# Kernel tuning notes

Measured on AMD Instinct MI355X. Metric: run time of the kernel, lower is better.

## Reference

```python
import jax, jax.numpy as jnp
import numpy as np

LENGTH = 512
Q = 2 * LENGTH + 3  # num_states = 2*length + 3
ALPHA = 26          # amino-acid alphabet size
BATCH = 256
T = 512


def setup_inputs() -> dict:
    key = jax.random.key(0)
    k1, k2, k3, k4 = jax.random.split(key, 4)
    x = jax.random.randint(k1, (BATCH, T), 0, ALPHA, dtype=jnp.int32)
    A_logits = jax.random.normal(k2, (Q, Q), dtype=jnp.float32)
    B_logits = jax.random.normal(k3, (Q, ALPHA), dtype=jnp.float32)
    init_logits = jax.random.normal(k4, (Q,), dtype=jnp.float32)
    return {"x": x, "A_logits": A_logits, "B_logits": B_logits, "init_logits": init_logits}


def reference(x, A_logits, B_logits, init_logits):
    # Build stochastic matrices (as emitter/transitioner do from their kernels).
    A = jax.nn.softmax(A_logits, axis=-1)        # (q, q) row-stochastic transitions
    B = jax.nn.softmax(B_logits, axis=-1)        # (q, alpha) emission distributions
    init = jax.nn.softmax(init_logits)           # (q,) initial distribution

    # Precompute per-position emission probs: E[b, t, :] = B[:, x[b, t]]
    E = B.T[x]                                   # (B, T, q)

    # First step (self.init branch): forward = E0 * initial distribution
    f0 = E[:, 0] * init[None, :]                 # (B, q)
    S0 = jnp.sum(f0, axis=-1, keepdims=True)     # (B, 1)
    ll0 = jnp.log(S0)
    f0 = f0 / S0

    def step(carry, Et):
        f, ll = carry
        fwd = Et * (f @ A)                       # emit * transition  (B, q)
        S = jnp.sum(fwd, axis=-1, keepdims=True)
        ll = ll + jnp.log(S)
        fwd = fwd / S
        return (fwd, ll), fwd

    (_, loglik), fwd_seq = jax.lax.scan(step, (f0, ll0), jnp.swapaxes(E[:, 1:], 0, 1))
    # fwd_seq: (T-1, B, q) -> full (B, T, q) with first step prepended
    forward = jnp.swapaxes(jnp.concatenate([f0[None], fwd_seq], axis=0), 0, 1)
    return forward, loglik
```

## Files before the change

### kernel.cpp

```cpp
#include <hip/hip_runtime.h>
#include <stdint.h>


#define Q     1027
#define TT    512
#define ALPH  26
#define KCH   33
#define NTILE 65
#define NCHK  (KCH*64)
#define GIMG  (NCHK*16)
#define NCL   16
#define WPC   16
#define MB    16

typedef short  short8  __attribute__((ext_vector_type(8)));
typedef float  floatx4 __attribute__((ext_vector_type(4)));
typedef int    intx4   __attribute__((ext_vector_type(4)));

static constexpr size_t al512(size_t x) { return (x + 511) & ~size_t(511); }
static constexpr size_t OFF_APACK = 0;
static constexpr size_t SZ_APACK  = (size_t)NTILE * KCH * 64 * 16;
static constexpr size_t OFF_BSOFT = al512(OFF_APACK + SZ_APACK);
static constexpr size_t SZ_BSOFT  = (size_t)Q * ALPH * 4;
static constexpr size_t OFF_INIT  = al512(OFF_BSOFT + SZ_BSOFT);
static constexpr size_t OFF_AMAX  = al512(OFF_INIT + Q * 4);
static constexpr size_t OFF_AINV  = al512(OFF_AMAX + Q * 4);
static constexpr size_t OFF_GEX   = al512(OFF_AINV + Q * 4);
static constexpr size_t SZ_GEX    = (size_t)NCL * 2 * GIMG;
static constexpr size_t OFF_SP    = al512(OFF_GEX + SZ_GEX);
static constexpr size_t SZ_SP     = (size_t)NCL * 2 * 64 * MB * 4;
static constexpr size_t OFF_FLAGS = al512(OFF_SP + SZ_SP);
static constexpr size_t SZ_FLAGS  = (size_t)NCL * 64 * 4;
static constexpr size_t WS_NEED   = OFF_FLAGS + SZ_FLAGS;
static constexpr size_t FWDSZ     = (size_t)256 * TT * Q;

__device__ __forceinline__ uint32_t f2bf(float f) {
  uint32_t u = __float_as_uint(f);
  return (u + 0x7fffu + ((u >> 16) & 1u)) >> 16;
}


__global__ void k_zero(char* __restrict__ ws) {
  const size_t n = (WS_NEED - OFF_GEX) / 16;
  intx4* p = (intx4*)(ws + OFF_GEX);
  for (size_t i = (size_t)blockIdx.x * 256 + threadIdx.x; i < n; i += (size_t)80 * 256)
    p[i] = intx4{0, 0, 0, 0};
}

__global__ void k_astats(const float* __restrict__ A, char* __restrict__ ws) {
  const int r = blockIdx.x, tid = threadIdx.x;
  const float* row = A + (size_t)r * Q;
  __shared__ float red[4], red2[4];
  float mx = -3.0e38f;
  for (int i = tid; i < Q; i += 256) mx = fmaxf(mx, row[i]);
#pragma unroll
  for (int d = 1; d < 64; d <<= 1) mx = fmaxf(mx, __shfl_xor(mx, d));
  if ((tid & 63) == 0) red[tid >> 6] = mx;
  __syncthreads();
  mx = fmaxf(fmaxf(red[0], red[1]), fmaxf(red[2], red[3]));
  float s = 0.f;
  for (int i = tid; i < Q; i += 256) s += expf(row[i] - mx);
#pragma unroll
  for (int d = 1; d < 64; d <<= 1) s += __shfl_xor(s, d);
  if ((tid & 63) == 0) red2[tid >> 6] = s;
  __syncthreads();
  s = red2[0] + red2[1] + red2[2] + red2[3];
  if (tid == 0) {
    *(float*)(ws + OFF_AMAX + (size_t)r * 4) = mx;
    *(float*)(ws + OFF_AINV + (size_t)r * 4) = 1.0f / s;
  }
}

__global__ void k_bsoft(const float* __restrict__ Bl, char* __restrict__ ws) {
  const int r = blockIdx.x, l = threadIdx.x;
  float v = (l < ALPH) ? Bl[(size_t)r * ALPH + l] : -3.0e38f;
  float mx = v;
#pragma unroll
  for (int d = 1; d < 64; d <<= 1) mx = fmaxf(mx, __shfl_xor(mx, d));
  float e = (l < ALPH) ? expf(v - mx) : 0.f;
  float s = e;
#pragma unroll
  for (int d = 1; d < 64; d <<= 1) s += __shfl_xor(s, d);
  if (l < ALPH) *(float*)(ws + OFF_BSOFT + ((size_t)r * ALPH + l) * 4) = e / s;
}

__global__ void k_isoft(const float* __restrict__ il, char* __restrict__ ws) {
  const int tid = threadIdx.x;
  __shared__ float red[4], red2[4];
  float mx = -3.0e38f;
  for (int i = tid; i < Q; i += 256) mx = fmaxf(mx, il[i]);
#pragma unroll
  for (int d = 1; d < 64; d <<= 1) mx = fmaxf(mx, __shfl_xor(mx, d));
  if ((tid & 63) == 0) red[tid >> 6] = mx;
  __syncthreads();
  mx = fmaxf(fmaxf(red[0], red[1]), fmaxf(red[2], red[3]));
  float s = 0.f;
  for (int i = tid; i < Q; i += 256) s += expf(il[i] - mx);
#pragma unroll
  for (int d = 1; d < 64; d <<= 1) s += __shfl_xor(s, d);
  if ((tid & 63) == 0) red2[tid >> 6] = s;
  __syncthreads();
  s = red2[0] + red2[1] + red2[2] + red2[3];
  const float inv = 1.0f / s;
  for (int i = tid; i < Q; i += 256)
    *(float*)(ws + OFF_INIT + (size_t)i * 4) = expf(il[i] - mx) * inv;
}

__global__ void k_repack(const float* __restrict__ A, char* __restrict__ ws) {
  const int b = blockIdx.x;
  const int nt = b % NTILE, kc = b / NTILE;
  const int lane = threadIdx.x;
  const int q = nt * 16 + (lane & 15);
  const int kb = kc * 32 + (lane >> 4) * 8;
  union { short8 v; unsigned short u[8]; } pk;
#pragma unroll
  for (int e = 0; e < 8; ++e) {
    const int k = kb + e;
    float val = 0.f;
    if (k < Q && q < Q) {
      const float mxk = *(const float*)(ws + OFF_AMAX + (size_t)k * 4);
      const float ivk = *(const float*)(ws + OFF_AINV + (size_t)k * 4);
      val = expf(A[(size_t)k * Q + q] - mxk) * ivk;
    }
    pk.u[e] = (unsigned short)f2bf(val);
  }
  *(short8*)(ws + OFF_APACK + (((size_t)nt * KCH + kc) * 64 + lane) * 16) = pk.v;
}


__global__ __launch_bounds__(256, 1) void k_main(const int* __restrict__ xin,
                                                 char* __restrict__ ws,
                                                 float* __restrict__ out) {
  const int bid = blockIdx.x;
  const int c = bid & 15, j = bid >> 4;
  const int tid = threadIdx.x;
  const int lane = tid & 63, w = tid >> 6;
  const int cL = lane & 15, g4 = lane >> 4;
  const int tg = 4 * j + w;
  const bool jx = (j == 15), two = (jx && w == 3);
  const uint64_t wsu = (uint64_t)(uintptr_t)ws;

  __shared__ floatx4 accx[4][5][64];
  __shared__ uint8_t x_lds[MB * TT];
  __shared__ float   B_lds[5][16][ALPH];
  __shared__ float   init_lds[5][16];
  __shared__ float   SpW[4][16];

  for (int idx = tid; idx < MB * TT; idx += 256)
    x_lds[idx] = (uint8_t)xin[(size_t)(c * MB) * TT + idx];
  for (int idx = tid; idx < 5 * 16 * ALPH; idx += 256) {
    const int tl = idx / (16 * ALPH), rem = idx % (16 * ALPH);
    const int cc = rem / ALPH, a = rem % ALPH;
    const int grow = (tl < 4 ? 64 * j + tl * 16 : 1024) + cc;
    B_lds[tl][cc][a] = (grow < Q) ? *(const float*)(ws + OFF_BSOFT + ((size_t)grow * ALPH + a) * 4) : 0.f;
  }
  for (int idx = tid; idx < 5 * 16; idx += 256) {
    const int tl = idx / 16, cc = idx % 16;
    const int grow = (tl < 4 ? 64 * j + tl * 16 : 1024) + cc;
    init_lds[tl][cc] = (grow < Q) ? *(const float*)(ws + OFF_INIT + (size_t)grow * 4) : 0.f;
  }

  short8 af[4][9];
#pragma unroll
  for (int tt = 0; tt < 4; ++tt)
#pragma unroll
    for (int i = 0; i < 9; ++i)
      if (i < 8 || w == 0)
        af[tt][i] = *(const short8*)(ws + OFF_APACK +
                      (((size_t)(4 * j + tt) * KCH + (4 * i + w)) * 64 + lane) * 16);
  short8 afx[9];
  if (jx) {
#pragma unroll
    for (int i = 0; i < 9; ++i)
      if (i < 8 || w == 0)
        afx[i] = *(const short8*)(ws + OFF_APACK +
                      (((size_t)64 * KCH + (4 * i + w)) * 64 + lane) * 16);
  }
  __syncthreads();

  float up0[4], upx[4] = {0.f, 0.f, 0.f, 0.f};
  float uold[4], uxold[4] = {0.f, 0.f, 0.f, 0.f};
  float llacc = 0.f;

#define POST_STEP(TCUR)                                                                   \
  do {                                                                                    \
    const int par_ = (TCUR) & 1;                                                          \
    const uint64_t gb_ = wsu + OFF_GEX + (size_t)(c * 2 + par_) * GIMG;                   \
    const uint64_t b0_ = gb_ + (size_t)((tg >> 1) * 1024 + ((tg & 1) * 2 + (cL >> 3)) * 256 \
                         + g4 * 64 + (cL & 7) * 2);                                       \
    float t0_ = up0[0], t1_ = up0[1], t2_ = up0[2], t3_ = up0[3];                         \
    _Pragma("unroll") for (int r = 0; r < 4; ++r) {                                       \
      uint32_t v0_ = f2bf(up0[r]);                                                        \
      asm volatile("global_store_short %0, %1, off sc0 sc1" ::                            \
                   "v"(b0_ + (size_t)(r * 16)), "v"(v0_) : "memory");                     \
    }                                                                                     \
    if (two) {                                                                            \
      const uint64_t bx_ = gb_ + (size_t)(32 * 1024 + (cL >> 3) * 256 + g4 * 64 +         \
                           (cL & 7) * 2);                                                 \
      _Pragma("unroll") for (int r = 0; r < 4; ++r) {                                     \
        uint32_t v1_ = f2bf(upx[r]);                                                      \
        asm volatile("global_store_short %0, %1, off sc0 sc1" ::                          \
                     "v"(bx_ + (size_t)(r * 16)), "v"(v1_) : "memory");                   \
      }                                                                                   \
      t0_ += upx[0]; t1_ += upx[1]; t2_ += upx[2]; t3_ += upx[3];                         \
    }                                                                                     \
    _Pragma("unroll") for (int d = 1; d < 16; d <<= 1) {                                  \
      t0_ += __shfl_xor(t0_, d); t1_ += __shfl_xor(t1_, d);                               \
      t2_ += __shfl_xor(t2_, d); t3_ += __shfl_xor(t3_, d);                               \
    }                                                                                     \
    if (cL == 0) {                                                                        \
      floatx4 sv_; sv_[0] = t0_; sv_[1] = t1_; sv_[2] = t2_; sv_[3] = t3_;                \
      uint64_t sa_ = wsu + OFF_SP + (size_t)(c * 2 + par_) * 4096 +                       \
                     (size_t)(tg * 64 + g4 * 16);                                         \
      asm volatile("global_store_dwordx4 %0, %1, off sc0 sc1" :: "v"(sa_), "v"(sv_)       \
                   : "memory");                                                           \
    }                                                                                     \
    asm volatile("s_waitcnt vmcnt(0)" ::: "memory");                                      \
    __builtin_amdgcn_sched_barrier(0);                                                    \
    if (lane == 0) {                                                                      \
      int fv_ = (TCUR) + 1;                                                               \
      asm volatile("global_store_dword %0, %1, off sc0 sc1" ::                            \
                   "v"(wsu + OFF_FLAGS + (size_t)(c * 64 + tg) * 4), "v"(fv_) : "memory");\
    }                                                                                     \
  } while (0)

#define WAIT_FLAGS(TGT)                                                                   \
  do {                                                                                    \
    if (w == 0) {                                                                         \
      const uint64_t fa_ = wsu + OFF_FLAGS + (size_t)(c * 64 + lane) * 4;                 \
      for (;;) {                                                                          \
        int f_;                                                                           \
        asm volatile("global_load_dword %0, %1, off sc0 sc1\n\ts_waitcnt vmcnt(0)"        \
                     : "=v"(f_) : "v"(fa_) : "memory");                                   \
        if (__all(f_ >= (TGT))) break;                                                    \
        __builtin_amdgcn_s_sleep(2);                                                      \
      }                                                                                   \
    }                                                                                     \
    __syncthreads();                                                                      \
  } while (0)

#pragma unroll
  for (int r = 0; r < 4; ++r) {
    const int m = g4 * 4 + r;
    const int xm = x_lds[m * TT + 0];
    up0[r] = B_lds[w][cL][xm] * init_lds[w][cL];
    uold[r] = up0[r];
    if (two) { upx[r] = B_lds[4][cL][xm] * init_lds[4][cL]; uxold[r] = upx[r]; }
  }
  POST_STEP(0);

  for (int t = 1; t < TT; ++t) {
    const int parp = (t - 1) & 1;
    WAIT_FLAGS(t);

    const uint64_t gb = wsu + OFF_GEX + (size_t)(c * 2 + parp) * GIMG;
    intx4 sg[9], spi;
#pragma unroll
    for (int i = 0; i < 8; ++i)
      asm volatile("global_load_dwordx4 %0, %1, off sc0 sc1"
                   : "=v"(sg[i]) : "v"(gb + (size_t)((i * 256 + tid) * 16)) : "memory");
    if (w == 0)
      asm volatile("global_load_dwordx4 %0, %1, off sc0 sc1"
                   : "=v"(sg[8]) : "v"(gb + (size_t)((2048 + lane) * 16)) : "memory");
    asm volatile("global_load_dwordx4 %0, %1, off sc0 sc1"
                 : "=v"(spi)
                 : "v"(wsu + OFF_SP + (size_t)(c * 2 + parp) * 4096 + (size_t)tid * 16)
                 : "memory");
    asm volatile("s_waitcnt vmcnt(1)" ::: "memory");
    __builtin_amdgcn_sched_barrier(0);

    floatx4 acc[4] = {{0,0,0,0},{0,0,0,0},{0,0,0,0},{0,0,0,0}};
    floatx4 acx = {0, 0, 0, 0};
#pragma unroll
    for (int i = 0; i < 8; ++i) {
      const short8 gf = __builtin_bit_cast(short8, sg[i]);
#pragma unroll
      for (int tt = 0; tt < 4; ++tt)
        acc[tt] = __builtin_amdgcn_mfma_f32_16x16x32_bf16(gf, af[tt][i], acc[tt], 0, 0, 0);
      if (jx) acx = __builtin_amdgcn_mfma_f32_16x16x32_bf16(gf, afx[i], acx, 0, 0, 0);
    }
    if (w == 0) {
      const short8 gf = __builtin_bit_cast(short8, sg[8]);
#pragma unroll
      for (int tt = 0; tt < 4; ++tt)
        acc[tt] = __builtin_amdgcn_mfma_f32_16x16x32_bf16(gf, af[tt][8], acc[tt], 0, 0, 0);
      if (jx) acx = __builtin_amdgcn_mfma_f32_16x16x32_bf16(gf, afx[8], acx, 0, 0, 0);
    }
#pragma unroll
    for (int tt = 0; tt < 4; ++tt) accx[w][tt][lane] = acc[tt];
    if (jx) accx[w][4][lane] = acx;

    asm volatile("s_waitcnt vmcnt(0)" ::: "memory");
    __builtin_amdgcn_sched_barrier(0);
    floatx4 s4 = __builtin_bit_cast(floatx4, spi);
#pragma unroll
    for (int d = 4; d < 64; d <<= 1) {
#pragma unroll
      for (int e = 0; e < 4; ++e) s4[e] += __shfl_xor(s4[e], d);
    }
    if (lane < 4) *(floatx4*)&SpW[w][lane * 4] = s4;
    __syncthreads();

    float invS[4], ot0[4], ot1[4];
    floatx4 rs = accx[0][w][lane] + accx[1][w][lane] + accx[2][w][lane] + accx[3][w][lane];
    float rx[4];
    if (two) {
      floatx4 q = accx[0][4][lane] + accx[1][4][lane] + accx[2][4][lane] + accx[3][4][lane];
#pragma unroll
      for (int r = 0; r < 4; ++r) rx[r] = q[r];
    }
#pragma unroll
    for (int r = 0; r < 4; ++r) {
      const int m = g4 * 4 + r;
      invS[r] = 1.0f / (SpW[0][m] + SpW[1][m] + SpW[2][m] + SpW[3][m]);
      ot0[r] = uold[r] * invS[r];
      if (two) ot1[r] = uxold[r] * invS[r];
      const int xm = x_lds[m * TT + t];
      up0[r] = rs[r] * B_lds[w][cL][xm] * invS[r];
      uold[r] = up0[r];
      if (two) { upx[r] = rx[r] * B_lds[4][cL][xm] * invS[r]; uxold[r] = upx[r]; }
    }

    POST_STEP(t);

#pragma unroll
    for (int r = 0; r < 4; ++r) {
      const int m = g4 * 4 + r;
      const size_t ob = ((size_t)(c * MB + m) * TT + (t - 1)) * Q;
      __builtin_nontemporal_store(ot0[r], out + ob + tg * 16 + cL);
      if (two && cL < 3)
        __builtin_nontemporal_store(ot1[r], out + ob + 1024 + cL);
    }
    if (j == 0 && w == 0 && lane < 16)
      llacc += logf(SpW[0][lane] + SpW[1][lane] + SpW[2][lane] + SpW[3][lane]);
  }

  WAIT_FLAGS(TT);
  {
    const int parp = (TT - 1) & 1;
    intx4 spi;
    asm volatile("global_load_dwordx4 %0, %1, off sc0 sc1\n\ts_waitcnt vmcnt(0)"
                 : "=v"(spi)
                 : "v"(wsu + OFF_SP + (size_t)(c * 2 + parp) * 4096 + (size_t)tid * 16)
                 : "memory");
    __builtin_amdgcn_sched_barrier(0);
    floatx4 s4 = __builtin_bit_cast(floatx4, spi);
#pragma unroll
    for (int d = 4; d < 64; d <<= 1) {
#pragma unroll
      for (int e = 0; e < 4; ++e) s4[e] += __shfl_xor(s4[e], d);
    }
    if (lane < 4) *(floatx4*)&SpW[w][lane * 4] = s4;
    __syncthreads();
    float invS[4];
#pragma unroll
    for (int r = 0; r < 4; ++r) {
      const int m = g4 * 4 + r;
      invS[r] = 1.0f / (SpW[0][m] + SpW[1][m] + SpW[2][m] + SpW[3][m]);
    }
#pragma unroll
    for (int r = 0; r < 4; ++r) {
      const int m = g4 * 4 + r;
      const size_t ob = ((size_t)(c * MB + m) * TT + (TT - 1)) * Q;
      __builtin_nontemporal_store(up0[r] * invS[r], out + ob + tg * 16 + cL);
      if (two && cL < 3)
        __builtin_nontemporal_store(upx[r] * invS[r], out + ob + 1024 + cL);
    }
    if (j == 0 && w == 0 && lane < 16) {
      llacc += logf(SpW[0][lane] + SpW[1][lane] + SpW[2][lane] + SpW[3][lane]);
      out[FWDSZ + (size_t)c * MB + lane] = llacc;
    }
  }
}


extern "C" void kernel_launch(void* const* d_in, const int* in_sizes, int n_in,
                              void* d_out, int out_size, void* d_ws, size_t ws_size,
                              hipStream_t stream) {
  const int*   x    = (const int*)d_in[0];
  const float* Alog = (const float*)d_in[1];
  const float* Blog = (const float*)d_in[2];
  const float* ilog = (const float*)d_in[3];
  char*  ws  = (char*)d_ws;
  float* out = (float*)d_out;
  if (ws_size < WS_NEED) return;

  hipLaunchKernelGGL(k_zero,   dim3(80),          dim3(256), 0, stream, ws);
  hipLaunchKernelGGL(k_astats, dim3(Q),           dim3(256), 0, stream, Alog, ws);
  hipLaunchKernelGGL(k_bsoft,  dim3(Q),           dim3(64),  0, stream, Blog, ws);
  hipLaunchKernelGGL(k_isoft,  dim3(1),           dim3(256), 0, stream, ilog, ws);
  hipLaunchKernelGGL(k_repack, dim3(NTILE * KCH), dim3(64),  0, stream, Alog, ws);
  hipLaunchKernelGGL(k_main,   dim3(NCL * WPC),   dim3(256), 0, stream, x, ws, out);
}
```

Baseline: 2.152 ms.

## Derive row sums from the exchanged state buffer and prefetch flags early

Drops the separate per-tile partial-sum buffer and its global store and load. Each block now recomputes the normalisation sums by adding up the bf16 state vector it already loads from the exchange buffer. The flag poll is issued right after publishing, overlapping its latency, and the sleep is removed from the spin loop. This trims one global round trip and some cross-block traffic per step. In exchange it adds per-step unpacking arithmetic and sums rounded bf16 values instead of fp32 partials, which may change the normaliser slightly.

```diff
diff --git a/kernel.cpp b/kernel.cpp
--- a/kernel.cpp
+++ b/kernel.cpp
@@ -27,9 +27,7 @@
 static constexpr size_t OFF_AINV  = al512(OFF_AMAX + Q * 4);
 static constexpr size_t OFF_GEX   = al512(OFF_AINV + Q * 4);
 static constexpr size_t SZ_GEX    = (size_t)NCL * 2 * GIMG;
-static constexpr size_t OFF_SP    = al512(OFF_GEX + SZ_GEX);
-static constexpr size_t SZ_SP     = (size_t)NCL * 2 * 64 * MB * 4;
-static constexpr size_t OFF_FLAGS = al512(OFF_SP + SZ_SP);
+static constexpr size_t OFF_FLAGS = al512(OFF_GEX + SZ_GEX);
 static constexpr size_t SZ_FLAGS  = (size_t)NCL * 64 * 4;
 static constexpr size_t WS_NEED   = OFF_FLAGS + SZ_FLAGS;
 static constexpr size_t FWDSZ     = (size_t)256 * TT * Q;
@@ -39,11 +37,22 @@
   return (u + 0x7fffu + ((u >> 16) & 1u)) >> 16;
 }
 
+__device__ __forceinline__ float sum8(intx4 v) {
+  float s = 0.f;
+#pragma unroll
+  for (int e = 0; e < 4; ++e) {
+    const uint32_t u = (uint32_t)v[e];
+    s += __uint_as_float(u << 16);
+    s += __uint_as_float(u & 0xffff0000u);
+  }
+  return s;
+}
+
 
 __global__ void k_zero(char* __restrict__ ws) {
   const size_t n = (WS_NEED - OFF_GEX) / 16;
   intx4* p = (intx4*)(ws + OFF_GEX);
-  for (size_t i = (size_t)blockIdx.x * 256 + threadIdx.x; i < n; i += (size_t)80 * 256)
+  for (size_t i = (size_t)blockIdx.x * 256 + threadIdx.x; i < n; i += (size_t)72 * 256)
     p[i] = intx4{0, 0, 0, 0};
 }
 
@@ -139,12 +148,13 @@
   const int tg = 4 * j + w;
   const bool jx = (j == 15), two = (jx && w == 3);
   const uint64_t wsu = (uint64_t)(uintptr_t)ws;
+  const uint64_t outu = (uint64_t)(uintptr_t)out;
 
   __shared__ floatx4 accx[4][5][64];
   __shared__ uint8_t x_lds[MB * TT];
   __shared__ float   B_lds[5][16][ALPH];
   __shared__ float   init_lds[5][16];
-  __shared__ float   SpW[4][16];
+  __shared__ float   SpP[4][16];
 
   for (int idx = tid; idx < MB * TT; idx += 256)
     x_lds[idx] = (uint8_t)xin[(size_t)(c * MB) * TT + idx];
@@ -181,63 +191,31 @@
   float up0[4], upx[4] = {0.f, 0.f, 0.f, 0.f};
   float uold[4], uxold[4] = {0.f, 0.f, 0.f, 0.f};
   float llacc = 0.f;
-
-#define POST_STEP(TCUR)                                                                   \
+  const uint64_t fa = wsu + OFF_FLAGS + (size_t)(c * 64 + lane) * 4;
+  const uint64_t myfa = wsu + OFF_FLAGS + (size_t)(c * 64 + tg) * 4;
+
+#define POSTG(TCUR)                                                                       \
   do {                                                                                    \
     const int par_ = (TCUR) & 1;                                                          \
     const uint64_t gb_ = wsu + OFF_GEX + (size_t)(c * 2 + par_) * GIMG;                   \
     const uint64_t b0_ = gb_ + (size_t)((tg >> 1) * 1024 + ((tg & 1) * 2 + (cL >> 3)) * 256 \
                          + g4 * 64 + (cL & 7) * 2);                                       \
-    float t0_ = up0[0], t1_ = up0[1], t2_ = up0[2], t3_ = up0[3];                         \
-    _Pragma("unroll") for (int r = 0; r < 4; ++r) {                                       \
-      uint32_t v0_ = f2bf(up0[r]);                                                        \
+    _Pragma("unroll") for (int r_ = 0; r_ < 4; ++r_) {                                    \
+      uint32_t v_ = f2bf(up0[r_]);                                                        \
       asm volatile("global_store_short %0, %1, off sc0 sc1" ::                            \
-                   "v"(b0_ + (size_t)(r * 16)), "v"(v0_) : "memory");                     \
+                   "v"(b0_ + (size_t)(r_ * 16)), "v"(v_) : "memory");                     \
     }                                                                                     \
     if (two) {                                                                            \
-      const uint64_t bx_ = gb_ + (size_t)(32 * 1024 + (cL >> 3) * 256 + g4 * 64 +         \
-                           (cL & 7) * 2);                                                 \
-      _Pragma("unroll") for (int r = 0; r < 4; ++r) {                                     \
-        uint32_t v1_ = f2bf(upx[r]);                                                      \
+      const uint64_t bx_ = gb_ + (size_t)(32 * 1024 + (cL >> 3) * 256 + g4 * 64 + (cL & 7) * 2); \
+      _Pragma("unroll") for (int r_ = 0; r_ < 4; ++r_) {                                  \
+        uint32_t v_ = f2bf(upx[r_]);                                                      \
         asm volatile("global_store_short %0, %1, off sc0 sc1" ::                          \
-                     "v"(bx_ + (size_t)(r * 16)), "v"(v1_) : "memory");                   \
+                     "v"(bx_ + (size_t)(r_ * 16)), "v"(v_) : "memory");                   \
       }                                                                                   \
-      t0_ += upx[0]; t1_ += upx[1]; t2_ += upx[2]; t3_ += upx[3];                         \
-    }                                                                                     \
-    _Pragma("unroll") for (int d = 1; d < 16; d <<= 1) {                                  \
-      t0_ += __shfl_xor(t0_, d); t1_ += __shfl_xor(t1_, d);                               \
-      t2_ += __shfl_xor(t2_, d); t3_ += __shfl_xor(t3_, d);                               \
-    }                                                                                     \
-    if (cL == 0) {                                                                        \
-      floatx4 sv_; sv_[0] = t0_; sv_[1] = t1_; sv_[2] = t2_; sv_[3] = t3_;                \
-      uint64_t sa_ = wsu + OFF_SP + (size_t)(c * 2 + par_) * 4096 +                       \
-                     (size_t)(tg * 64 + g4 * 16);                                         \
-      asm volatile("global_store_dwordx4 %0, %1, off sc0 sc1" :: "v"(sa_), "v"(sv_)       \
-                   : "memory");                                                           \
-    }                                                                                     \
-    asm volatile("s_waitcnt vmcnt(0)" ::: "memory");                                      \
-    __builtin_amdgcn_sched_barrier(0);                                                    \
-    if (lane == 0) {                                                                      \
-      int fv_ = (TCUR) + 1;                                                               \
-      asm volatile("global_store_dword %0, %1, off sc0 sc1" ::                            \
-                   "v"(wsu + OFF_FLAGS + (size_t)(c * 64 + tg) * 4), "v"(fv_) : "memory");\
     }                                                                                     \
   } while (0)
 
-#define WAIT_FLAGS(TGT)                                                                   \
-  do {                                                                                    \
-    if (w == 0) {                                                                         \
-      const uint64_t fa_ = wsu + OFF_FLAGS + (size_t)(c * 64 + lane) * 4;                 \
-      for (;;) {                                                                          \
-        int f_;                                                                           \
-        asm volatile("global_load_dword %0, %1, off sc0 sc1\n\ts_waitcnt vmcnt(0)"        \
-                     : "=v"(f_) : "v"(fa_) : "memory");                                   \
-        if (__all(f_ >= (TGT))) break;                                                    \
-        __builtin_amdgcn_s_sleep(2);                                                      \
-      }                                                                                   \
-    }                                                                                     \
-    __syncthreads();                                                                      \
-  } while (0)
+  int f;
 
 #pragma unroll
   for (int r = 0; r < 4; ++r) {
@@ -247,14 +225,27 @@
     uold[r] = up0[r];
     if (two) { upx[r] = B_lds[4][cL][xm] * init_lds[4][cL]; uxold[r] = upx[r]; }
   }
-  POST_STEP(0);
+  POSTG(0);
+  asm volatile("global_load_dword %0, %1, off sc0 sc1" : "=v"(f) : "v"(fa) : "memory");
+  asm volatile("s_waitcnt vmcnt(0)" ::: "memory");
+  __builtin_amdgcn_sched_barrier(0);
+  if (lane == 0) {
+    int fv = 1;
+    asm volatile("global_store_dword %0, %1, off sc0 sc1" :: "v"(myfa), "v"(fv) : "memory");
+  }
 
   for (int t = 1; t < TT; ++t) {
     const int parp = (t - 1) & 1;
-    WAIT_FLAGS(t);
+
+    for (;;) {
+      if (__all(f >= t)) break;
+      asm volatile("global_load_dword %0, %1, off sc0 sc1\n\ts_waitcnt vmcnt(0)"
+                   : "=v"(f) : "v"(fa) : "memory");
+    }
+    __builtin_amdgcn_sched_barrier(0);
 
     const uint64_t gb = wsu + OFF_GEX + (size_t)(c * 2 + parp) * GIMG;
-    intx4 sg[9], spi;
+    intx4 sg[9];
 #pragma unroll
     for (int i = 0; i < 8; ++i)
       asm volatile("global_load_dwordx4 %0, %1, off sc0 sc1"
@@ -262,12 +253,16 @@
     if (w == 0)
       asm volatile("global_load_dwordx4 %0, %1, off sc0 sc1"
                    : "=v"(sg[8]) : "v"(gb + (size_t)((2048 + lane) * 16)) : "memory");
-    asm volatile("global_load_dwordx4 %0, %1, off sc0 sc1"
-                 : "=v"(spi)
-                 : "v"(wsu + OFF_SP + (size_t)(c * 2 + parp) * 4096 + (size_t)tid * 16)
-                 : "memory");
-    asm volatile("s_waitcnt vmcnt(1)" ::: "memory");
+    asm volatile("s_waitcnt vmcnt(0)" ::: "memory");
     __builtin_amdgcn_sched_barrier(0);
+
+    float ps = 0.f;
+#pragma unroll
+    for (int i = 0; i < 8; ++i) ps += sum8(sg[i]);
+    if (w == 0) ps += sum8(sg[8]);
+    ps += __shfl_xor(ps, 16);
+    ps += __shfl_xor(ps, 32);
+    if (lane < 16) SpP[w][lane] = ps;
 
     floatx4 acc[4] = {{0,0,0,0},{0,0,0,0},{0,0,0,0},{0,0,0,0}};
     floatx4 acx = {0, 0, 0, 0};
@@ -290,15 +285,6 @@
     for (int tt = 0; tt < 4; ++tt) accx[w][tt][lane] = acc[tt];
     if (jx) accx[w][4][lane] = acx;
 
-    asm volatile("s_waitcnt vmcnt(0)" ::: "memory");
-    __builtin_amdgcn_sched_barrier(0);
-    floatx4 s4 = __builtin_bit_cast(floatx4, spi);
-#pragma unroll
-    for (int d = 4; d < 64; d <<= 1) {
-#pragma unroll
-      for (int e = 0; e < 4; ++e) s4[e] += __shfl_xor(s4[e], d);
-    }
-    if (lane < 4) *(floatx4*)&SpW[w][lane * 4] = s4;
     __syncthreads();
 
     float invS[4], ot0[4], ot1[4];
@@ -309,10 +295,12 @@
 #pragma unroll
       for (int r = 0; r < 4; ++r) rx[r] = q[r];
     }
+    float llS = 1.f;
+    if (lane < 16) llS = SpP[0][lane] + SpP[1][lane] + SpP[2][lane] + SpP[3][lane];
 #pragma unroll
     for (int r = 0; r < 4; ++r) {
       const int m = g4 * 4 + r;
-      invS[r] = 1.0f / (SpW[0][m] + SpW[1][m] + SpW[2][m] + SpW[3][m]);
+      invS[r] = 1.0f / (SpP[0][m] + SpP[1][m] + SpP[2][m] + SpP[3][m]);
       ot0[r] = uold[r] * invS[r];
       if (two) ot1[r] = uxold[r] * invS[r];
       const int xm = x_lds[m * TT + t];
@@ -321,7 +309,14 @@
       if (two) { upx[r] = rx[r] * B_lds[4][cL][xm] * invS[r]; uxold[r] = upx[r]; }
     }
 
-    POST_STEP(t);
+    POSTG(t);
+    asm volatile("global_load_dword %0, %1, off sc0 sc1" : "=v"(f) : "v"(fa) : "memory");
+    asm volatile("s_waitcnt vmcnt(0)" ::: "memory");
+    __builtin_amdgcn_sched_barrier(0);
+    if (lane == 0) {
+      int fv = t + 1;
+      asm volatile("global_store_dword %0, %1, off sc0 sc1" :: "v"(myfa), "v"(fv) : "memory");
+    }
 
 #pragma unroll
     for (int r = 0; r < 4; ++r) {
@@ -331,32 +326,43 @@
       if (two && cL < 3)
         __builtin_nontemporal_store(ot1[r], out + ob + 1024 + cL);
     }
-    if (j == 0 && w == 0 && lane < 16)
-      llacc += logf(SpW[0][lane] + SpW[1][lane] + SpW[2][lane] + SpW[3][lane]);
-  }
-
-  WAIT_FLAGS(TT);
+    if (j == 0 && w == 0 && lane < 16) llacc += logf(llS);
+  }
+
+  for (;;) {
+    if (__all(f >= TT)) break;
+    asm volatile("global_load_dword %0, %1, off sc0 sc1\n\ts_waitcnt vmcnt(0)"
+                 : "=v"(f) : "v"(fa) : "memory");
+  }
+  __builtin_amdgcn_sched_barrier(0);
   {
     const int parp = (TT - 1) & 1;
-    intx4 spi;
-    asm volatile("global_load_dwordx4 %0, %1, off sc0 sc1\n\ts_waitcnt vmcnt(0)"
-                 : "=v"(spi)
-                 : "v"(wsu + OFF_SP + (size_t)(c * 2 + parp) * 4096 + (size_t)tid * 16)
-                 : "memory");
+    const uint64_t gb = wsu + OFF_GEX + (size_t)(c * 2 + parp) * GIMG;
+    intx4 sg[9];
+#pragma unroll
+    for (int i = 0; i < 8; ++i)
+      asm volatile("global_load_dwordx4 %0, %1, off sc0 sc1"
+                   : "=v"(sg[i]) : "v"(gb + (size_t)((i * 256 + tid) * 16)) : "memory");
+    if (w == 0)
+      asm volatile("global_load_dwordx4 %0, %1, off sc0 sc1"
+                   : "=v"(sg[8]) : "v"(gb + (size_t)((2048 + lane) * 16)) : "memory");
+    asm volatile("s_waitcnt vmcnt(0)" ::: "memory");
     __builtin_amdgcn_sched_barrier(0);
-    floatx4 s4 = __builtin_bit_cast(floatx4, spi);
-#pragma unroll
-    for (int d = 4; d < 64; d <<= 1) {
-#pragma unroll
-      for (int e = 0; e < 4; ++e) s4[e] += __shfl_xor(s4[e], d);
-    }
-    if (lane < 4) *(floatx4*)&SpW[w][lane * 4] = s4;
+    float ps = 0.f;
+#pragma unroll
+    for (int i = 0; i < 8; ++i) ps += sum8(sg[i]);
+    if (w == 0) ps += sum8(sg[8]);
+    ps += __shfl_xor(ps, 16);
+    ps += __shfl_xor(ps, 32);
+    if (lane < 16) SpP[w][lane] = ps;
     __syncthreads();
     float invS[4];
+    float llS = 1.f;
+    if (lane < 16) llS = SpP[0][lane] + SpP[1][lane] + SpP[2][lane] + SpP[3][lane];
 #pragma unroll
     for (int r = 0; r < 4; ++r) {
       const int m = g4 * 4 + r;
-      invS[r] = 1.0f / (SpW[0][m] + SpW[1][m] + SpW[2][m] + SpW[3][m]);
+      invS[r] = 1.0f / (SpP[0][m] + SpP[1][m] + SpP[2][m] + SpP[3][m]);
     }
 #pragma unroll
     for (int r = 0; r < 4; ++r) {
@@ -367,7 +373,7 @@
         __builtin_nontemporal_store(upx[r] * invS[r], out + ob + 1024 + cL);
     }
     if (j == 0 && w == 0 && lane < 16) {
-      llacc += logf(SpW[0][lane] + SpW[1][lane] + SpW[2][lane] + SpW[3][lane]);
+      llacc += logf(llS);
       out[FWDSZ + (size_t)c * MB + lane] = llacc;
     }
   }
@@ -385,7 +391,7 @@
   float* out = (float*)d_out;
   if (ws_size < WS_NEED) return;
 
-  hipLaunchKernelGGL(k_zero,   dim3(80),          dim3(256), 0, stream, ws);
+  hipLaunchKernelGGL(k_zero,   dim3(72),          dim3(256), 0, stream, ws);
   hipLaunchKernelGGL(k_astats, dim3(Q),           dim3(256), 0, stream, Alog, ws);
   hipLaunchKernelGGL(k_bsoft,  dim3(Q),           dim3(64),  0, stream, Blog, ws);
   hipLaunchKernelGGL(k_isoft,  dim3(1),           dim3(256), 0, stream, ilog, ws);
```

Result: slower. 4.840 ms (+125.0%).

## Replace block-wide flag wait with per-wave group flag polling

Applied to the files above, without the earlier changes.

Each wave now polls only the 16 producer flags matching its own K-chunk range of the shared vector, in place of wave 0 polling all 64 flags and then a block barrier. The K-chunk assignment per wave changes from interleaved to contiguous (8*w+i) so each wave's loads depend on one group of producers, and the tail chunk moves to wave 3. A __syncthreads is added after the LDS reads so the SpW and accx buffers are not overwritten early, and the log-likelihood sum is read before that barrier. The aim is to let waves start their MFMA work as soon as their own inputs are ready, cutting cross-block synchronisation latency, at the cost of more polling traffic.

```diff
diff --git a/kernel.cpp b/kernel.cpp
--- a/kernel.cpp
+++ b/kernel.cpp
@@ -138,6 +138,7 @@
   const int cL = lane & 15, g4 = lane >> 4;
   const int tg = 4 * j + w;
   const bool jx = (j == 15), two = (jx && w == 3);
+  const bool wt = (w == 3);
   const uint64_t wsu = (uint64_t)(uintptr_t)ws;
 
   __shared__ floatx4 accx[4][5][64];
@@ -165,22 +166,24 @@
   for (int tt = 0; tt < 4; ++tt)
 #pragma unroll
     for (int i = 0; i < 9; ++i)
-      if (i < 8 || w == 0)
+      if (i < 8 || wt)
         af[tt][i] = *(const short8*)(ws + OFF_APACK +
-                      (((size_t)(4 * j + tt) * KCH + (4 * i + w)) * 64 + lane) * 16);
+                      (((size_t)(4 * j + tt) * KCH + (8 * w + i)) * 64 + lane) * 16);
   short8 afx[9];
   if (jx) {
 #pragma unroll
     for (int i = 0; i < 9; ++i)
-      if (i < 8 || w == 0)
+      if (i < 8 || wt)
         afx[i] = *(const short8*)(ws + OFF_APACK +
-                      (((size_t)64 * KCH + (4 * i + w)) * 64 + lane) * 16);
+                      (((size_t)64 * KCH + (8 * w + i)) * 64 + lane) * 16);
   }
   __syncthreads();
 
   float up0[4], upx[4] = {0.f, 0.f, 0.f, 0.f};
   float uold[4], uxold[4] = {0.f, 0.f, 0.f, 0.f};
   float llacc = 0.f;
+  const uint64_t fa = wsu + OFF_FLAGS + (size_t)(c * 64 + 16 * w + (lane & 15)) * 4;
+  const uint64_t myfa = wsu + OFF_FLAGS + (size_t)(c * 64 + tg) * 4;
 
 #define POST_STEP(TCUR)                                                                   \
   do {                                                                                    \
@@ -189,18 +192,17 @@
     const uint64_t b0_ = gb_ + (size_t)((tg >> 1) * 1024 + ((tg & 1) * 2 + (cL >> 3)) * 256 \
                          + g4 * 64 + (cL & 7) * 2);                                       \
     float t0_ = up0[0], t1_ = up0[1], t2_ = up0[2], t3_ = up0[3];                         \
-    _Pragma("unroll") for (int r = 0; r < 4; ++r) {                                       \
-      uint32_t v0_ = f2bf(up0[r]);                                                        \
+    _Pragma("unroll") for (int r_ = 0; r_ < 4; ++r_) {                                    \
+      uint32_t v_ = f2bf(up0[r_]);                                                        \
       asm volatile("global_store_short %0, %1, off sc0 sc1" ::                            \
-                   "v"(b0_ + (size_t)(r * 16)), "v"(v0_) : "memory");                     \
+                   "v"(b0_ + (size_t)(r_ * 16)), "v"(v_) : "memory");                     \
     }                                                                                     \
     if (two) {                                                                            \
-      const uint64_t bx_ = gb_ + (size_t)(32 * 1024 + (cL >> 3) * 256 + g4 * 64 +         \
-                           (cL & 7) * 2);                                                 \
-      _Pragma("unroll") for (int r = 0; r < 4; ++r) {                                     \
-        uint32_t v1_ = f2bf(upx[r]);                                                      \
+      const uint64_t bx_ = gb_ + (size_t)(32 * 1024 + (cL >> 3) * 256 + g4 * 64 + (cL & 7) * 2); \
+      _Pragma("unroll") for (int r_ = 0; r_ < 4; ++r_) {                                  \
+        uint32_t v_ = f2bf(upx[r_]);                                                      \
         asm volatile("global_store_short %0, %1, off sc0 sc1" ::                          \
-                     "v"(bx_ + (size_t)(r * 16)), "v"(v1_) : "memory");                   \
+                     "v"(bx_ + (size_t)(r_ * 16)), "v"(v_) : "memory");                   \
       }                                                                                   \
       t0_ += upx[0]; t1_ += upx[1]; t2_ += upx[2]; t3_ += upx[3];                         \
     }                                                                                     \
@@ -219,24 +221,21 @@
     __builtin_amdgcn_sched_barrier(0);                                                    \
     if (lane == 0) {                                                                      \
       int fv_ = (TCUR) + 1;                                                               \
-      asm volatile("global_store_dword %0, %1, off sc0 sc1" ::                            \
-                   "v"(wsu + OFF_FLAGS + (size_t)(c * 64 + tg) * 4), "v"(fv_) : "memory");\
+      asm volatile("global_store_dword %0, %1, off sc0 sc1" :: "v"(myfa), "v"(fv_)        \
+                   : "memory");                                                           \
     }                                                                                     \
   } while (0)
 
-#define WAIT_FLAGS(TGT)                                                                   \
+#define WAIT_GRP(TGT)                                                                     \
   do {                                                                                    \
-    if (w == 0) {                                                                         \
-      const uint64_t fa_ = wsu + OFF_FLAGS + (size_t)(c * 64 + lane) * 4;                 \
-      for (;;) {                                                                          \
-        int f_;                                                                           \
-        asm volatile("global_load_dword %0, %1, off sc0 sc1\n\ts_waitcnt vmcnt(0)"        \
-                     : "=v"(f_) : "v"(fa_) : "memory");                                   \
-        if (__all(f_ >= (TGT))) break;                                                    \
-        __builtin_amdgcn_s_sleep(2);                                                      \
-      }                                                                                   \
-    }                                                                                     \
-    __syncthreads();                                                                      \
+    for (;;) {                                                                            \
+      int f_;                                                                             \
+      asm volatile("global_load_dword %0, %1, off sc0 sc1\n\ts_waitcnt vmcnt(0)"          \
+                   : "=v"(f_) : "v"(fa) : "memory");                                      \
+      if (__all(f_ >= (TGT))) break;                                                      \
+      __builtin_amdgcn_s_sleep(1);                                                        \
+    }                                                                                     \
+    __builtin_amdgcn_sched_barrier(0);                                                    \
   } while (0)
 
 #pragma unroll
@@ -251,15 +250,16 @@
 
   for (int t = 1; t < TT; ++t) {
     const int parp = (t - 1) & 1;
-    WAIT_FLAGS(t);
+
+    WAIT_GRP(t);
 
     const uint64_t gb = wsu + OFF_GEX + (size_t)(c * 2 + parp) * GIMG;
     intx4 sg[9], spi;
 #pragma unroll
     for (int i = 0; i < 8; ++i)
       asm volatile("global_load_dwordx4 %0, %1, off sc0 sc1"
-                   : "=v"(sg[i]) : "v"(gb + (size_t)((i * 256 + tid) * 16)) : "memory");
-    if (w == 0)
+                   : "=v"(sg[i]) : "v"(gb + (size_t)((512 * w + 64 * i + lane) * 16)) : "memory");
+    if (wt)
       asm volatile("global_load_dwordx4 %0, %1, off sc0 sc1"
                    : "=v"(sg[8]) : "v"(gb + (size_t)((2048 + lane) * 16)) : "memory");
     asm volatile("global_load_dwordx4 %0, %1, off sc0 sc1"
@@ -279,7 +279,7 @@
         acc[tt] = __builtin_amdgcn_mfma_f32_16x16x32_bf16(gf, af[tt][i], acc[tt], 0, 0, 0);
       if (jx) acx = __builtin_amdgcn_mfma_f32_16x16x32_bf16(gf, afx[i], acx, 0, 0, 0);
     }
-    if (w == 0) {
+    if (wt) {
       const short8 gf = __builtin_bit_cast(short8, sg[8]);
 #pragma unroll
       for (int tt = 0; tt < 4; ++tt)
@@ -309,6 +309,8 @@
 #pragma unroll
       for (int r = 0; r < 4; ++r) rx[r] = q[r];
     }
+    float llS = 1.f;
+    if (lane < 16) llS = SpW[0][lane] + SpW[1][lane] + SpW[2][lane] + SpW[3][lane];
 #pragma unroll
     for (int r = 0; r < 4; ++r) {
       const int m = g4 * 4 + r;
@@ -320,6 +322,7 @@
       uold[r] = up0[r];
       if (two) { upx[r] = rx[r] * B_lds[4][cL][xm] * invS[r]; uxold[r] = upx[r]; }
     }
+    __syncthreads();
 
     POST_STEP(t);
 
@@ -331,11 +334,10 @@
       if (two && cL < 3)
         __builtin_nontemporal_store(ot1[r], out + ob + 1024 + cL);
     }
-    if (j == 0 && w == 0 && lane < 16)
-      llacc += logf(SpW[0][lane] + SpW[1][lane] + SpW[2][lane] + SpW[3][lane]);
-  }
-
-  WAIT_FLAGS(TT);
+    if (j == 0 && w == 0 && lane < 16) llacc += logf(llS);
+  }
+
+  WAIT_GRP(TT);
   {
     const int parp = (TT - 1) & 1;
     intx4 spi;
@@ -353,6 +355,8 @@
     if (lane < 4) *(floatx4*)&SpW[w][lane * 4] = s4;
     __syncthreads();
     float invS[4];
+    float llS = 1.f;
+    if (lane < 16) llS = SpW[0][lane] + SpW[1][lane] + SpW[2][lane] + SpW[3][lane];
 #pragma unroll
     for (int r = 0; r < 4; ++r) {
       const int m = g4 * 4 + r;
@@ -367,7 +371,7 @@
         __builtin_nontemporal_store(upx[r] * invS[r], out + ob + 1024 + cL);
     }
     if (j == 0 && w == 0 && lane < 16) {
-      llacc += logf(SpW[0][lane] + SpW[1][lane] + SpW[2][lane] + SpW[3][lane]);
+      llacc += logf(llS);
       out[FWDSZ + (size_t)c * MB + lane] = llacc;
     }
   }
```

After: 2.436 ms. 13.2% more time.

## Probe cache coherence at runtime and use cheaper sc0-only cross-block sync

Applied to the files above, without the earlier changes.

Adds a runtime handshake in which the 16 blocks of each cluster write magic values with sc0-only stores and check whether peers can read them. If every block sees them, the main loop is instantiated with sc0-only loads and stores (dropping sc1) and a shorter spin sleep, to cut the latency of per-step inter-block exchange and flag polling. Otherwise it falls back to the original sc0 sc1 path. It costs an extra startup barrier plus a larger workspace, and correctness depends on the probe reliably showing that the blocks share a coherent cache level.

```diff
diff --git a/kernel.cpp b/kernel.cpp
--- a/kernel.cpp
+++ b/kernel.cpp
@@ -31,12 +31,40 @@
 static constexpr size_t SZ_SP     = (size_t)NCL * 2 * 64 * MB * 4;
 static constexpr size_t OFF_FLAGS = al512(OFF_SP + SZ_SP);
 static constexpr size_t SZ_FLAGS  = (size_t)NCL * 64 * 4;
-static constexpr size_t WS_NEED   = OFF_FLAGS + SZ_FLAGS;
+static constexpr size_t OFF_TEST  = al512(OFF_FLAGS + SZ_FLAGS);
+static constexpr size_t OFF_TFLG  = al512(OFF_TEST + 4096);
+static constexpr size_t OFF_OKF   = al512(OFF_TFLG + 4096);
+static constexpr size_t WS_NEED   = OFF_OKF + 4096;
 static constexpr size_t FWDSZ     = (size_t)256 * TT * Q;
 
 __device__ __forceinline__ uint32_t f2bf(float f) {
   uint32_t u = __float_as_uint(f);
   return (u + 0x7fffu + ((u >> 16) & 1u)) >> 16;
+}
+
+template <bool DEV> __device__ __forceinline__ void st2(uint64_t a, uint32_t v) {
+  if constexpr (DEV) asm volatile("global_store_short %0, %1, off sc0 sc1" :: "v"(a), "v"(v) : "memory");
+  else               asm volatile("global_store_short %0, %1, off sc0"     :: "v"(a), "v"(v) : "memory");
+}
+template <bool DEV> __device__ __forceinline__ void st4(uint64_t a, int v) {
+  if constexpr (DEV) asm volatile("global_store_dword %0, %1, off sc0 sc1" :: "v"(a), "v"(v) : "memory");
+  else               asm volatile("global_store_dword %0, %1, off sc0"     :: "v"(a), "v"(v) : "memory");
+}
+template <bool DEV> __device__ __forceinline__ void st16(uint64_t a, floatx4 v) {
+  if constexpr (DEV) asm volatile("global_store_dwordx4 %0, %1, off sc0 sc1" :: "v"(a), "v"(v) : "memory");
+  else               asm volatile("global_store_dwordx4 %0, %1, off sc0"     :: "v"(a), "v"(v) : "memory");
+}
+template <bool DEV> __device__ __forceinline__ intx4 ld16(uint64_t a) {
+  intx4 r;
+  if constexpr (DEV) asm volatile("global_load_dwordx4 %0, %1, off sc0 sc1" : "=v"(r) : "v"(a) : "memory");
+  else               asm volatile("global_load_dwordx4 %0, %1, off sc0"     : "=v"(r) : "v"(a) : "memory");
+  return r;
+}
+template <bool DEV> __device__ __forceinline__ int ld4w(uint64_t a) {
+  int r;
+  if constexpr (DEV) asm volatile("global_load_dword %0, %1, off sc0 sc1\n\ts_waitcnt vmcnt(0)" : "=v"(r) : "v"(a) : "memory");
+  else               asm volatile("global_load_dword %0, %1, off sc0\n\ts_waitcnt vmcnt(0)"     : "=v"(r) : "v"(a) : "memory");
+  return r;
 }
 
 
@@ -128,37 +156,20 @@
 }
 
 
-__global__ __launch_bounds__(256, 1) void k_main(const int* __restrict__ xin,
-                                                 char* __restrict__ ws,
-                                                 float* __restrict__ out) {
-  const int bid = blockIdx.x;
-  const int c = bid & 15, j = bid >> 4;
+template <bool DEV>
+__device__ __forceinline__ void hmm_run(char* __restrict__ ws, float* __restrict__ out,
+                                        int c, int j,
+                                        uint8_t (&x_lds)[MB * TT],
+                                        float (&B_lds)[5][16][ALPH],
+                                        float (&init_lds)[5][16],
+                                        floatx4 (&accx)[4][5][64],
+                                        float (&SpW)[4][16]) {
   const int tid = threadIdx.x;
   const int lane = tid & 63, w = tid >> 6;
   const int cL = lane & 15, g4 = lane >> 4;
   const int tg = 4 * j + w;
   const bool jx = (j == 15), two = (jx && w == 3);
   const uint64_t wsu = (uint64_t)(uintptr_t)ws;
-
-  __shared__ floatx4 accx[4][5][64];
-  __shared__ uint8_t x_lds[MB * TT];
-  __shared__ float   B_lds[5][16][ALPH];
-  __shared__ float   init_lds[5][16];
-  __shared__ float   SpW[4][16];
-
-  for (int idx = tid; idx < MB * TT; idx += 256)
-    x_lds[idx] = (uint8_t)xin[(size_t)(c * MB) * TT + idx];
-  for (int idx = tid; idx < 5 * 16 * ALPH; idx += 256) {
-    const int tl = idx / (16 * ALPH), rem = idx % (16 * ALPH);
-    const int cc = rem / ALPH, a = rem % ALPH;
-    const int grow = (tl < 4 ? 64 * j + tl * 16 : 1024) + cc;
-    B_lds[tl][cc][a] = (grow < Q) ? *(const float*)(ws + OFF_BSOFT + ((size_t)grow * ALPH + a) * 4) : 0.f;
-  }
-  for (int idx = tid; idx < 5 * 16; idx += 256) {
-    const int tl = idx / 16, cc = idx % 16;
-    const int grow = (tl < 4 ? 64 * j + tl * 16 : 1024) + cc;
-    init_lds[tl][cc] = (grow < Q) ? *(const float*)(ws + OFF_INIT + (size_t)grow * 4) : 0.f;
-  }
 
   short8 af[4][9];
 #pragma unroll
@@ -189,19 +200,12 @@
     const uint64_t b0_ = gb_ + (size_t)((tg >> 1) * 1024 + ((tg & 1) * 2 + (cL >> 3)) * 256 \
                          + g4 * 64 + (cL & 7) * 2);                                       \
     float t0_ = up0[0], t1_ = up0[1], t2_ = up0[2], t3_ = up0[3];                         \
-    _Pragma("unroll") for (int r = 0; r < 4; ++r) {                                       \
-      uint32_t v0_ = f2bf(up0[r]);                                                        \
-      asm volatile("global_store_short %0, %1, off sc0 sc1" ::                            \
-                   "v"(b0_ + (size_t)(r * 16)), "v"(v0_) : "memory");                     \
-    }                                                                                     \
+    _Pragma("unroll") for (int r_ = 0; r_ < 4; ++r_)                                      \
+      st2<DEV>(b0_ + (size_t)(r_ * 16), f2bf(up0[r_]));                                   \
     if (two) {                                                                            \
-      const uint64_t bx_ = gb_ + (size_t)(32 * 1024 + (cL >> 3) * 256 + g4 * 64 +         \
-                           (cL & 7) * 2);                                                 \
-      _Pragma("unroll") for (int r = 0; r < 4; ++r) {                                     \
-        uint32_t v1_ = f2bf(upx[r]);                                                      \
-        asm volatile("global_store_short %0, %1, off sc0 sc1" ::                          \
-                     "v"(bx_ + (size_t)(r * 16)), "v"(v1_) : "memory");                   \
-      }                                                                                   \
+      const uint64_t bx_ = gb_ + (size_t)(32 * 1024 + (cL >> 3) * 256 + g4 * 64 + (cL & 7) * 2); \
+      _Pragma("unroll") for (int r_ = 0; r_ < 4; ++r_)                                    \
+        st2<DEV>(bx_ + (size_t)(r_ * 16), f2bf(upx[r_]));                                 \
       t0_ += upx[0]; t1_ += upx[1]; t2_ += upx[2]; t3_ += upx[3];                         \
     }                                                                                     \
     _Pragma("unroll") for (int d = 1; d < 16; d <<= 1) {                                  \
@@ -210,18 +214,12 @@
     }                                                                                     \
     if (cL == 0) {                                                                        \
       floatx4 sv_; sv_[0] = t0_; sv_[1] = t1_; sv_[2] = t2_; sv_[3] = t3_;                \
-      uint64_t sa_ = wsu + OFF_SP + (size_t)(c * 2 + par_) * 4096 +                       \
-                     (size_t)(tg * 64 + g4 * 16);                                         \
-      asm volatile("global_store_dwordx4 %0, %1, off sc0 sc1" :: "v"(sa_), "v"(sv_)       \
-                   : "memory");                                                           \
+      st16<DEV>(wsu + OFF_SP + (size_t)(c * 2 + par_) * 4096 + (size_t)(tg * 64 + g4 * 16), sv_); \
     }                                                                                     \
     asm volatile("s_waitcnt vmcnt(0)" ::: "memory");                                      \
     __builtin_amdgcn_sched_barrier(0);                                                    \
-    if (lane == 0) {                                                                      \
-      int fv_ = (TCUR) + 1;                                                               \
-      asm volatile("global_store_dword %0, %1, off sc0 sc1" ::                            \
-                   "v"(wsu + OFF_FLAGS + (size_t)(c * 64 + tg) * 4), "v"(fv_) : "memory");\
-    }                                                                                     \
+    if (lane == 0)                                                                        \
+      st4<DEV>(wsu + OFF_FLAGS + (size_t)(c * 64 + tg) * 4, (TCUR) + 1);                  \
   } while (0)
 
 #define WAIT_FLAGS(TGT)                                                                   \
@@ -229,11 +227,10 @@
     if (w == 0) {                                                                         \
       const uint64_t fa_ = wsu + OFF_FLAGS + (size_t)(c * 64 + lane) * 4;                 \
       for (;;) {                                                                          \
-        int f_;                                                                           \
-        asm volatile("global_load_dword %0, %1, off sc0 sc1\n\ts_waitcnt vmcnt(0)"        \
-                     : "=v"(f_) : "v"(fa_) : "memory");                                   \
+        int f_ = ld4w<DEV>(fa_);                                                          \
         if (__all(f_ >= (TGT))) break;                                                    \
-        __builtin_amdgcn_s_sleep(2);                                                      \
+        if constexpr (DEV) __builtin_amdgcn_s_sleep(2);                                   \
+        else               __builtin_amdgcn_s_sleep(1);                                   \
       }                                                                                   \
     }                                                                                     \
     __syncthreads();                                                                      \
@@ -257,15 +254,10 @@
     intx4 sg[9], spi;
 #pragma unroll
     for (int i = 0; i < 8; ++i)
-      asm volatile("global_load_dwordx4 %0, %1, off sc0 sc1"
-                   : "=v"(sg[i]) : "v"(gb + (size_t)((i * 256 + tid) * 16)) : "memory");
+      sg[i] = ld16<DEV>(gb + (size_t)((i * 256 + tid) * 16));
     if (w == 0)
-      asm volatile("global_load_dwordx4 %0, %1, off sc0 sc1"
-                   : "=v"(sg[8]) : "v"(gb + (size_t)((2048 + lane) * 16)) : "memory");
-    asm volatile("global_load_dwordx4 %0, %1, off sc0 sc1"
-                 : "=v"(spi)
-                 : "v"(wsu + OFF_SP + (size_t)(c * 2 + parp) * 4096 + (size_t)tid * 16)
-                 : "memory");
+      sg[8] = ld16<DEV>(gb + (size_t)((2048 + lane) * 16));
+    spi = ld16<DEV>(wsu + OFF_SP + (size_t)(c * 2 + parp) * 4096 + (size_t)tid * 16);
     asm volatile("s_waitcnt vmcnt(1)" ::: "memory");
     __builtin_amdgcn_sched_barrier(0);
 
@@ -309,6 +301,8 @@
 #pragma unroll
       for (int r = 0; r < 4; ++r) rx[r] = q[r];
     }
+    float llS = 1.f;
+    if (lane < 16) llS = SpW[0][lane] + SpW[1][lane] + SpW[2][lane] + SpW[3][lane];
 #pragma unroll
     for (int r = 0; r < 4; ++r) {
       const int m = g4 * 4 + r;
@@ -331,18 +325,14 @@
       if (two && cL < 3)
         __builtin_nontemporal_store(ot1[r], out + ob + 1024 + cL);
     }
-    if (j == 0 && w == 0 && lane < 16)
-      llacc += logf(SpW[0][lane] + SpW[1][lane] + SpW[2][lane] + SpW[3][lane]);
+    if (j == 0 && w == 0 && lane < 16) llacc += logf(llS);
   }
 
   WAIT_FLAGS(TT);
   {
     const int parp = (TT - 1) & 1;
-    intx4 spi;
-    asm volatile("global_load_dwordx4 %0, %1, off sc0 sc1\n\ts_waitcnt vmcnt(0)"
-                 : "=v"(spi)
-                 : "v"(wsu + OFF_SP + (size_t)(c * 2 + parp) * 4096 + (size_t)tid * 16)
-                 : "memory");
+    intx4 spi = ld16<DEV>(wsu + OFF_SP + (size_t)(c * 2 + parp) * 4096 + (size_t)tid * 16);
+    asm volatile("s_waitcnt vmcnt(0)" ::: "memory");
     __builtin_amdgcn_sched_barrier(0);
     floatx4 s4 = __builtin_bit_cast(floatx4, spi);
 #pragma unroll
@@ -353,6 +343,8 @@
     if (lane < 4) *(floatx4*)&SpW[w][lane * 4] = s4;
     __syncthreads();
     float invS[4];
+    float llS = 1.f;
+    if (lane < 16) llS = SpW[0][lane] + SpW[1][lane] + SpW[2][lane] + SpW[3][lane];
 #pragma unroll
     for (int r = 0; r < 4; ++r) {
       const int m = g4 * 4 + r;
@@ -367,10 +359,88 @@
         __builtin_nontemporal_store(upx[r] * invS[r], out + ob + 1024 + cL);
     }
     if (j == 0 && w == 0 && lane < 16) {
-      llacc += logf(SpW[0][lane] + SpW[1][lane] + SpW[2][lane] + SpW[3][lane]);
+      llacc += logf(llS);
       out[FWDSZ + (size_t)c * MB + lane] = llacc;
     }
   }
+#undef POST_STEP
+#undef WAIT_FLAGS
+}
+
+
+__global__ __launch_bounds__(256, 1) void k_main(const int* __restrict__ xin,
+                                                 char* __restrict__ ws,
+                                                 float* __restrict__ out) {
+  const int bid = blockIdx.x;
+  const int c = bid & 15, j = bid >> 4;
+  const int tid = threadIdx.x;
+  const int lane = tid & 63, w = tid >> 6;
+  const int tg = 4 * j + w;
+  const uint64_t wsu = (uint64_t)(uintptr_t)ws;
+
+  __shared__ floatx4 accx[4][5][64];
+  __shared__ uint8_t x_lds[MB * TT];
+  __shared__ float   B_lds[5][16][ALPH];
+  __shared__ float   init_lds[5][16];
+  __shared__ float   SpW[4][16];
+
+  for (int idx = tid; idx < MB * TT; idx += 256)
+    x_lds[idx] = (uint8_t)xin[(size_t)(c * MB) * TT + idx];
+  for (int idx = tid; idx < 5 * 16 * ALPH; idx += 256) {
+    const int tl = idx / (16 * ALPH), rem = idx % (16 * ALPH);
+    const int cc = rem / ALPH, a = rem % ALPH;
+    const int grow = (tl < 4 ? 64 * j + tl * 16 : 1024) + cc;
+    B_lds[tl][cc][a] = (grow < Q) ? *(const float*)(ws + OFF_BSOFT + ((size_t)grow * ALPH + a) * 4) : 0.f;
+  }
+  for (int idx = tid; idx < 5 * 16; idx += 256) {
+    const int tl = idx / 16, cc = idx % 16;
+    const int grow = (tl < 4 ? 64 * j + tl * 16 : 1024) + cc;
+    init_lds[tl][cc] = (grow < Q) ? *(const float*)(ws + OFF_INIT + (size_t)grow * 4) : 0.f;
+  }
+
+  bool pure;
+  {
+    const uint64_t ta  = wsu + OFF_TEST + (size_t)(c * 64 + tg) * 4;
+    const uint64_t tfa = wsu + OFF_TFLG + (size_t)(c * 64 + tg) * 4;
+    const uint64_t pta = wsu + OFF_TEST + (size_t)(c * 64 + lane) * 4;
+    const uint64_t pfa = wsu + OFF_TFLG + (size_t)(c * 64 + lane) * 4;
+    bool ok = true;
+    int gate = 0;
+#pragma unroll 1
+    for (int ph = 0; ph < 2; ++ph) {
+      const int magic = 0x5A100000 + ph * 0x10000;
+      if (lane == 0) {
+        asm volatile("global_store_dword %0, %1, off sc0" :: "v"(ta), "v"(magic + tg) : "memory");
+        asm volatile("s_waitcnt vmcnt(0)" ::: "memory");
+        st4<true>(tfa, ++gate);
+      } else { ++gate; }
+      for (;;) {
+        int fv = ld4w<true>(pfa);
+        if (__all(fv >= gate)) break;
+        __builtin_amdgcn_s_sleep(2);
+      }
+      int tv;
+      asm volatile("global_load_dword %0, %1, off sc0\n\ts_waitcnt vmcnt(0)" : "=v"(tv) : "v"(pta) : "memory");
+      ok = ok && __all(tv == magic + (int)lane);
+      if (lane == 0) st4<true>(tfa, ++gate); else ++gate;
+      for (;;) {
+        int fv = ld4w<true>(pfa);
+        if (__all(fv >= gate)) break;
+        __builtin_amdgcn_s_sleep(2);
+      }
+    }
+    if (lane == 0) st4<true>(wsu + OFF_OKF + (size_t)(c * 64 + tg) * 4, ok ? 2 : 1);
+    int av;
+    for (;;) {
+      av = ld4w<true>(wsu + OFF_OKF + (size_t)(c * 64 + lane) * 4);
+      if (__all(av != 0)) break;
+      __builtin_amdgcn_s_sleep(2);
+    }
+    pure = __all(av == 2);
+  }
+
+  if (pure) hmm_run<false>(ws, out, c, j, x_lds, B_lds, init_lds, accx, SpW);
+  else      hmm_run<true>(ws, out, c, j, x_lds, B_lds, init_lds, accx, SpW);
 }
 
 
```

Result: slower. 2.305 ms (+7.1%).
